# Performance work log

Hardware: AMD Instinct MI355X
Metric: run time of the kernel (lower is better)

The kernel has to match this reference:

```python
import jax, jax.numpy as jnp
import numpy as np

B, S, D, H = 4, 2048, 512, 8
DH = D // H  # 64


def setup_inputs() -> dict:
    key = jax.random.key(0)
    ks = jax.random.split(key, 7)
    scale = 1.0 / np.sqrt(D)
    return {
        "in_query": jax.random.normal(ks[0], (B, S, D), dtype=jnp.float32),
        "in_key": jax.random.normal(ks[1], (B, S, D), dtype=jnp.float32),
        "in_value": jax.random.normal(ks[2], (B, S, D), dtype=jnp.float32),
        "W_q": jax.random.normal(ks[3], (D, D), dtype=jnp.float32) * scale,
        "W_k": jax.random.normal(ks[4], (D, D), dtype=jnp.float32) * scale,
        "W_v": jax.random.normal(ks[5], (D, D), dtype=jnp.float32) * scale,
        "W_out": jax.random.normal(ks[6], (D, D), dtype=jnp.float32) * scale,
    }


def _split_heads(x):
    # [B, S, D] -> [B, H, S, DH]
    return x.reshape(B, S, H, DH).transpose(0, 2, 1, 3)


def reference(in_query, in_key, in_value, W_q, W_k, W_v, W_out):
    q = _split_heads(in_query @ W_q)   # [B,H,S,DH]
    k = _split_heads(in_key @ W_k)
    v = _split_heads(in_value @ W_v)
    scores = jnp.einsum("bhqd,bhkd->bhqk", q, k) / jnp.sqrt(jnp.float32(DH))
    attn = jax.nn.softmax(scores, axis=-1)  # dropout p=0 -> identity
    out = jnp.einsum("bhqk,bhkd->bhqd", attn, v)  # [B,H,S,DH]
    out = out.transpose(0, 2, 1, 3).reshape(B, S, D)
    return out @ W_out
```

## Files before the change

### kernel.cpp

```cpp
#include <hip/hip_runtime.h>
#include <hip/hip_bf16.h>
#include <cstdint>
#include <cstddef>


typedef __bf16 bf16;
typedef __attribute__((ext_vector_type(8))) __bf16 bf16x8;
typedef __attribute__((ext_vector_type(4))) __bf16 bf16x4;
typedef __attribute__((ext_vector_type(4))) float floatx4;

#define MFMA16(a, b, c) __builtin_amdgcn_mfma_f32_16x16x32_bf16(a, b, c, 0, 0, 0)

#define GLD16(gp, lp)                                              \
  __builtin_amdgcn_global_load_lds(                                \
      (const __attribute__((address_space(1))) unsigned int*)(gp), \
      (__attribute__((address_space(3))) unsigned int*)(lp), 16, 0, 0)

__device__ __forceinline__ void split2(float x, bf16& hi, bf16& lo) {
  hi = (bf16)x;
  lo = (bf16)(x - (float)hi);
}

__global__ __launch_bounds__(256) void k_split_w(
    const float* __restrict__ Wq, const float* __restrict__ Wk,
    const float* __restrict__ Wv, const float* __restrict__ Wo,
    bf16* __restrict__ wt_hi, bf16* __restrict__ wt_lo) {
  __shared__ float tile[64][65];
  const int w = blockIdx.z;
  const float* W = (w == 0) ? Wq : (w == 1) ? Wk : (w == 2) ? Wv : Wo;
  const int kb = blockIdx.y * 64, nb = blockIdx.x * 64;
  const int tid = threadIdx.x;
  const int col = tid & 63, rbase = tid >> 6;
#pragma unroll
  for (int i = 0; i < 16; i++) {
    int row = rbase + i * 4;
    tile[row][col] = W[(size_t)(kb + row) * 512 + nb + col];
  }
  __syncthreads();
#pragma unroll
  for (int i = 0; i < 16; i++) {
    int nrow = rbase + i * 4;
    float v = tile[col][nrow];
    bf16 hi, lo;
    split2(v, hi, lo);
    size_t o = (size_t)w * 262144 + (size_t)(nb + nrow) * 512 + (kb + col);
    wt_hi[o] = hi;
    wt_lo[o] = lo;
  }
}

__global__ __launch_bounds__(256) void k_proj_qkv(
    const float* __restrict__ Xq, const float* __restrict__ Xk,
    const float* __restrict__ Xv,
    const bf16* __restrict__ wt_hi, const bf16* __restrict__ wt_lo,
    bf16* __restrict__ Q_hi, bf16* __restrict__ Q_lo,
    bf16* __restrict__ K, bf16* __restrict__ Vt) {
  const int P = blockIdx.x;
  const int c_all = P >> 5, within = P & 31;
  const int n_idx = within >> 3, i8 = within & 7;
  const int which = c_all >> 3;
  const int g = ((c_all & 7) << 3) | i8;
  const int m0 = g * 128, n0 = n_idx * 128;

  const float* X = (which == 0) ? Xq : (which == 1) ? Xk : Xv;
  const uint8_t* Bhb = (const uint8_t*)(wt_hi + (size_t)which * 262144);
  const uint8_t* Blb = (const uint8_t*)(wt_lo + (size_t)which * 262144);
  const uint8_t* Xb = (const uint8_t*)X;
  const int tid = threadIdx.x, wave = tid >> 6, lane = tid & 63;
  const int l15 = lane & 15, l4 = lane >> 4;
  const int Am0 = (wave & 1) * 64, Bn0 = (wave >> 1) * 64;

  __shared__ float sA[128 * 32];
  __shared__ bf16 sBh[128 * 32], sBl[128 * 32];

  int aoff[4], adst[4];
#pragma unroll
  for (int p = 0; p < 4; p++) {
    int slot = p * 256 + tid;
    int row = slot >> 3, phys = slot & 7, lg = phys ^ (row & 7);
    aoff[p] = (m0 + row) * 2048 + lg * 16;
    adst[p] = slot * 16;
  }
  int boff[2], bdst[2];
#pragma unroll
  for (int p = 0; p < 2; p++) {
    int slot = p * 256 + tid;
    int row = slot >> 2, phys = slot & 3, lg = phys ^ (row & 3);
    boff[p] = (n0 + row) * 1024 + lg * 16;
    bdst[p] = slot * 16;
  }

  floatx4 acc[4][4];
#pragma unroll
  for (int i = 0; i < 4; i++)
#pragma unroll
    for (int j = 0; j < 4; j++) acc[i][j] = {0.f, 0.f, 0.f, 0.f};

  for (int kb = 0; kb < 512; kb += 32) {
    __syncthreads();
#pragma unroll
    for (int p = 0; p < 4; p++) GLD16(Xb + aoff[p] + kb * 4, (char*)sA + adst[p]);
#pragma unroll
    for (int p = 0; p < 2; p++) {
      GLD16(Bhb + boff[p] + kb * 2, (char*)sBh + bdst[p]);
      GLD16(Blb + boff[p] + kb * 2, (char*)sBl + bdst[p]);
    }
    __syncthreads();

    bf16x8 ah[4], al[4];
#pragma unroll
    for (int mt = 0; mt < 4; mt++) {
      int row = Am0 + mt * 16 + l15, r7 = row & 7;
      const float* f0 = (const float*)((const char*)sA + row * 128 + (((2 * l4) ^ r7) * 16));
      const float* f1 = (const float*)((const char*)sA + row * 128 + (((2 * l4 + 1) ^ r7) * 16));
#pragma unroll
      for (int j = 0; j < 4; j++) {
        bf16 h, l;
        split2(f0[j], h, l);
        ah[mt][j] = h; al[mt][j] = l;
        split2(f1[j], h, l);
        ah[mt][4 + j] = h; al[mt][4 + j] = l;
      }
    }
#pragma unroll
    for (int nt = 0; nt < 4; nt++) {
      int row = Bn0 + nt * 16 + l15, r3 = row & 3;
      bf16x8 bh = *(const bf16x8*)((const char*)sBh + row * 64 + ((l4 ^ r3) * 16));
      bf16x8 bl = *(const bf16x8*)((const char*)sBl + row * 64 + ((l4 ^ r3) * 16));
#pragma unroll
      for (int mt = 0; mt < 4; mt++) {
        acc[mt][nt] = MFMA16(ah[mt], bh, acc[mt][nt]);
        acc[mt][nt] = MFMA16(ah[mt], bl, acc[mt][nt]);
        acc[mt][nt] = MFMA16(al[mt], bh, acc[mt][nt]);
      }
    }
  }

  const float scale = (which == 0) ? 0.125f : (which == 1) ? 1.44269504f : 1.0f;
#pragma unroll
  for (int mt = 0; mt < 4; mt++) {
#pragma unroll
    for (int nt = 0; nt < 4; nt++) {
      int m_base = m0 + Am0 + mt * 16 + l4 * 4;
      int n = n0 + Bn0 + nt * 16 + l15;
      int h = (n >> 6) & 7, d = n & 63;
      if (which == 2) {
        int kbase = m_base & 2047, b = m_base >> 11;
        int a32 = kbase & ~31, v = (kbase >> 2) & 7;
        int sbase = a32 + 8 * (v & 3) + 4 * (v >> 2);
        bf16x4 pv;
#pragma unroll
        for (int r = 0; r < 4; r++) pv[r] = (bf16)acc[mt][nt][r];
        *(bf16x4*)&Vt[((size_t)(b * 8 + h) * 64 + d) * 2048 + sbase] = pv;
      } else {
#pragma unroll
        for (int r = 0; r < 4; r++) {
          int m = m_base + r;
          int b = m >> 11, s = m & 2047;
          float v = acc[mt][nt][r] * scale;
          size_t o = ((size_t)(b * 8 + h) * 2048 + s) * 64 + d;
          if (which == 0) {
            bf16 hi, lo;
            split2(v, hi, lo);
            Q_hi[o] = hi; Q_lo[o] = lo;
          } else {
            K[o] = (bf16)v;
          }
        }
      }
    }
  }
}

__global__ __launch_bounds__(256, 2) void k_flash(
    const bf16* __restrict__ Q_hi, const bf16* __restrict__ Q_lo,
    const bf16* __restrict__ K, const bf16* __restrict__ Vt,
    bf16* __restrict__ O_hi, bf16* __restrict__ O_lo) {
  const int P = blockIdx.x;
  const int hi4 = P >> 8, rem = P & 255;
  const int qt = rem >> 3;
  const int bh = hi4 * 8 + (rem & 7);
  const int b = bh >> 3, h = bh & 7;
  const int tid = threadIdx.x, wave = tid >> 6, lane = tid & 63;
  const int l15 = lane & 15, l4 = lane >> 4;
  const int q0 = qt * 64;

  __shared__ char smem[33792];
  bf16* sK = (bf16*)smem;
  bf16* sV = (bf16*)(smem + 16384);
  float* lbuf = (float*)(smem + 32768);

  bf16x8 qh[4][2], ql[4][2];
#pragma unroll
  for (int nt = 0; nt < 4; nt++) {
    const bf16* ph = Q_hi + ((size_t)bh * 2048 + q0 + nt * 16 + l15) * 64 + l4 * 8;
    const bf16* pl = Q_lo + ((size_t)bh * 2048 + q0 + nt * 16 + l15) * 64 + l4 * 8;
    qh[nt][0] = *(const bf16x8*)ph;
    qh[nt][1] = *(const bf16x8*)(ph + 32);
    ql[nt][0] = *(const bf16x8*)pl;
    ql[nt][1] = *(const bf16x8*)(pl + 32);
  }

  const uint8_t* Kb = (const uint8_t*)K + (size_t)bh * 2048 * 128;
  const uint8_t* Vb = (const uint8_t*)Vt + (size_t)bh * 64 * 4096;
  int koff[4], voff[4], dst[4];
#pragma unroll
  for (int p = 0; p < 4; p++) {
    int slot = p * 256 + tid;
    {
      int row = slot >> 3, phys = slot & 7, lg = phys ^ (row & 7);
      koff[p] = row * 128 + lg * 16;
    }
    {
      int row = slot >> 4, phys = slot & 15, lg = phys ^ (row & 15);
      voff[p] = row * 4096 + lg * 16;
    }
    dst[p] = slot * 16;
  }

  float lp[4] = {0.f, 0.f, 0.f, 0.f};
  floatx4 oacc[4][4];
#pragma unroll
  for (int i = 0; i < 4; i++)
#pragma unroll
    for (int j = 0; j < 4; j++) oacc[i][j] = {0.f, 0.f, 0.f, 0.f};

  for (int j0 = 0; j0 < 2048; j0 += 128) {
    __syncthreads();
#pragma unroll
    for (int p = 0; p < 4; p++) {
      GLD16(Kb + (size_t)j0 * 128 + koff[p], (char*)sK + dst[p]);
      GLD16(Vb + (size_t)j0 * 2 + voff[p], (char*)sV + dst[p]);
    }
    __syncthreads();

    floatx4 sc[2][4];
#pragma unroll
    for (int kt = 0; kt < 2; kt++)
#pragma unroll
      for (int nt = 0; nt < 4; nt++)
        sc[kt][nt] = {-24.f, -24.f, -24.f, -24.f};
#pragma unroll
    for (int kt = 0; kt < 2; kt++) {
      int row = wave * 32 + kt * 16 + l15;
      int r7 = row & 7;
#pragma unroll
      for (int ks = 0; ks < 2; ks++) {
        bf16x8 kh = *(const bf16x8*)((const char*)sK +
                                     (row * 128 + (((ks * 4 + l4) ^ r7) * 16)));
#pragma unroll
        for (int nt = 0; nt < 4; nt++) {
          sc[kt][nt] = MFMA16(kh, qh[nt][ks], sc[kt][nt]);
          sc[kt][nt] = MFMA16(kh, ql[nt][ks], sc[kt][nt]);
        }
      }
    }

    bf16x8 pf[4];
#pragma unroll
    for (int nt = 0; nt < 4; nt++) {
#pragma unroll
      for (int r = 0; r < 4; r++) {
        float p0 = __builtin_amdgcn_exp2f(sc[0][nt][r]);
        float p1 = __builtin_amdgcn_exp2f(sc[1][nt][r]);
        lp[nt] += p0 + p1;
        pf[nt][r] = (bf16)p0;
        pf[nt][4 + r] = (bf16)p1;
      }
    }

#pragma unroll
    for (int nt = 0; nt < 4; nt++) {
      int row = nt * 16 + l15;
      bf16x8 bv = *(const bf16x8*)((const char*)sV +
                                   (row * 256 + (((wave * 4 + l4) ^ l15) * 16)));
#pragma unroll
      for (int mq = 0; mq < 4; mq++)
        oacc[mq][nt] = MFMA16(pf[mq], bv, oacc[mq][nt]);
    }
  }

#pragma unroll
  for (int nt = 0; nt < 4; nt++) {
    lp[nt] += __shfl_xor(lp[nt], 16, 64);
    lp[nt] += __shfl_xor(lp[nt], 32, 64);
  }
  __syncthreads();
  if (l4 == 0) {
#pragma unroll
    for (int nt = 0; nt < 4; nt++) lbuf[wave * 64 + nt * 16 + l15] = lp[nt];
  }
  floatx4* red = (floatx4*)smem;
#pragma unroll
  for (int phase = 0; phase < 2; phase++) {
    if (wave >= 1) {
#pragma unroll
      for (int i = 0; i < 8; i++) {
        int mq = phase * 2 + (i >> 2);
        red[(wave - 1) * 512 + i * 64 + lane] = oacc[mq][i & 3];
      }
    }
    __syncthreads();
    if (wave == 0) {
#pragma unroll
      for (int i = 0; i < 8; i++) {
        int mq = phase * 2 + (i >> 2);
        oacc[mq][i & 3] += red[i * 64 + lane] + red[512 + i * 64 + lane] +
                           red[1024 + i * 64 + lane];
      }
    }
    __syncthreads();
  }
  if (wave == 0) {
    float lt[4];
#pragma unroll
    for (int nt = 0; nt < 4; nt++)
      lt[nt] = lbuf[nt * 16 + l15] + lbuf[64 + nt * 16 + l15] +
               lbuf[128 + nt * 16 + l15] + lbuf[192 + nt * 16 + l15];
    float rl[4][4];
#pragma unroll
    for (int mq = 0; mq < 4; mq++)
#pragma unroll
      for (int r = 0; r < 4; r++)
        rl[mq][r] = 1.0f / __shfl(lt[mq], (lane & 48) | (l4 * 4 + r), 64);
#pragma unroll
    for (int mq = 0; mq < 4; mq++) {
#pragma unroll
      for (int nt = 0; nt < 4; nt++) {
#pragma unroll
        for (int r = 0; r < 4; r++) {
          float v = oacc[mq][nt][r] * rl[mq][r];
          int gs = q0 + mq * 16 + l4 * 4 + r;
          int gd = h * 64 + nt * 16 + l15;
          size_t o = ((size_t)b * 2048 + gs) * 512 + gd;
          bf16 hi, lo;
          split2(v, hi, lo);
          O_hi[o] = hi;
          O_lo[o] = lo;
        }
      }
    }
  }
}

__global__ __launch_bounds__(256) void k_proj_out(
    const bf16* __restrict__ O_hi, const bf16* __restrict__ O_lo,
    const bf16* __restrict__ wt_hi, const bf16* __restrict__ wt_lo,
    float* __restrict__ out) {
  const int P = blockIdx.x;
  const int c = P >> 5, within = P & 31;
  const int n_idx = within >> 3, i8 = within & 7;
  const int g = (c << 3) | i8;
  const int m0 = g * 128, n0 = n_idx * 128;

  const uint8_t* Ahb = (const uint8_t*)O_hi;
  const uint8_t* Alb = (const uint8_t*)O_lo;
  const uint8_t* Bhb = (const uint8_t*)(wt_hi + (size_t)3 * 262144);
  const uint8_t* Blb = (const uint8_t*)(wt_lo + (size_t)3 * 262144);
  const int tid = threadIdx.x, wave = tid >> 6, lane = tid & 63;
  const int l15 = lane & 15, l4 = lane >> 4;
  const int Am0 = (wave & 1) * 64, Bn0 = (wave >> 1) * 64;

  __shared__ bf16 sAh[128 * 32], sAl[128 * 32];
  __shared__ bf16 sBh[128 * 32], sBl[128 * 32];

  int aoff[2], boff[2], dst[2];
#pragma unroll
  for (int p = 0; p < 2; p++) {
    int slot = p * 256 + tid;
    int row = slot >> 2, phys = slot & 3, lg = phys ^ (row & 3);
    aoff[p] = (m0 + row) * 1024 + lg * 16;
    boff[p] = (n0 + row) * 1024 + lg * 16;
    dst[p] = slot * 16;
  }

  floatx4 acc[4][4];
#pragma unroll
  for (int i = 0; i < 4; i++)
#pragma unroll
    for (int j = 0; j < 4; j++) acc[i][j] = {0.f, 0.f, 0.f, 0.f};

  for (int kb = 0; kb < 512; kb += 32) {
    __syncthreads();
#pragma unroll
    for (int p = 0; p < 2; p++) {
      GLD16(Ahb + aoff[p] + kb * 2, (char*)sAh + dst[p]);
      GLD16(Alb + aoff[p] + kb * 2, (char*)sAl + dst[p]);
      GLD16(Bhb + boff[p] + kb * 2, (char*)sBh + dst[p]);
      GLD16(Blb + boff[p] + kb * 2, (char*)sBl + dst[p]);
    }
    __syncthreads();

    bf16x8 ah[4], al[4];
#pragma unroll
    for (int mt = 0; mt < 4; mt++) {
      int row = Am0 + mt * 16 + l15, r3 = row & 3;
      ah[mt] = *(const bf16x8*)((const char*)sAh + row * 64 + ((l4 ^ r3) * 16));
      al[mt] = *(const bf16x8*)((const char*)sAl + row * 64 + ((l4 ^ r3) * 16));
    }
#pragma unroll
    for (int nt = 0; nt < 4; nt++) {
      int row = Bn0 + nt * 16 + l15, r3 = row & 3;
      bf16x8 bh = *(const bf16x8*)((const char*)sBh + row * 64 + ((l4 ^ r3) * 16));
      bf16x8 bl = *(const bf16x8*)((const char*)sBl + row * 64 + ((l4 ^ r3) * 16));
#pragma unroll
      for (int mt = 0; mt < 4; mt++) {
        acc[mt][nt] = MFMA16(ah[mt], bh, acc[mt][nt]);
        acc[mt][nt] = MFMA16(ah[mt], bl, acc[mt][nt]);
        acc[mt][nt] = MFMA16(al[mt], bh, acc[mt][nt]);
      }
    }
  }
#pragma unroll
  for (int mt = 0; mt < 4; mt++) {
#pragma unroll
    for (int nt = 0; nt < 4; nt++) {
#pragma unroll
      for (int r = 0; r < 4; r++) {
        int m = m0 + Am0 + mt * 16 + l4 * 4 + r;
        int n = n0 + Bn0 + nt * 16 + l15;
        out[(size_t)m * 512 + n] = acc[mt][nt][r];
      }
    }
  }
}

extern "C" void kernel_launch(void* const* d_in, const int* in_sizes, int n_in,
                              void* d_out, int out_size, void* d_ws, size_t ws_size,
                              hipStream_t stream) {
  (void)in_sizes; (void)n_in; (void)out_size; (void)ws_size;
  const float* Xq = (const float*)d_in[0];
  const float* Xk = (const float*)d_in[1];
  const float* Xv = (const float*)d_in[2];
  const float* Wq = (const float*)d_in[3];
  const float* Wk = (const float*)d_in[4];
  const float* Wv = (const float*)d_in[5];
  const float* Wo = (const float*)d_in[6];
  float* out = (float*)d_out;

  char* ws = (char*)d_ws;
  size_t off = 0;
  auto alloc = [&](size_t n) {
    void* p = ws + off;
    off += (n + 255) & ~(size_t)255;
    return p;
  };
  const size_t NW = 4 * 262144;
  const size_t NE = 4194304;
  bf16* wt_hi = (bf16*)alloc(NW * 2);
  bf16* wt_lo = (bf16*)alloc(NW * 2);
  bf16* Qh = (bf16*)alloc(NE * 2);
  bf16* Ql = (bf16*)alloc(NE * 2);
  bf16* Kk = (bf16*)alloc(NE * 2);
  bf16* Vt = (bf16*)alloc(NE * 2);
  bf16* Oh = (bf16*)alloc(NE * 2);
  bf16* Ol = (bf16*)alloc(NE * 2);

  k_split_w<<<dim3(8, 8, 4), dim3(256), 0, stream>>>(Wq, Wk, Wv, Wo, wt_hi, wt_lo);
  k_proj_qkv<<<dim3(768), dim3(256), 0, stream>>>(Xq, Xk, Xv, wt_hi, wt_lo,
                                                  Qh, Ql, Kk, Vt);
  k_flash<<<dim3(1024), dim3(256), 0, stream>>>(Qh, Ql, Kk, Vt, Oh, Ol);
  k_proj_out<<<dim3(256), dim3(256), 0, stream>>>(Oh, Ol, wt_hi, wt_lo, out);
}
```

Before: 222.5 us.

## Double-buffer LDS tiles in projection and flash kernels to overlap loads

Adds a second shared-memory buffer to the QKV projection, flash attention and output projection kernels. The next K-slice or KV tile is prefetched with async global-to-LDS loads while the current tile is computed on, which removes one barrier per iteration and hides load latency. This doubles LDS use, and the flash kernel now needs about 65 KB per block, which may reduce occupancy. It also relies on the single trailing barrier to make the async LDS writes visible before the next iteration reads them.

```diff
diff --git a/kernel.cpp b/kernel.cpp
--- a/kernel.cpp
+++ b/kernel.cpp
@@ -49,7 +49,7 @@
   }
 }
 
-__global__ __launch_bounds__(256) void k_proj_qkv(
+__global__ __launch_bounds__(256, 2) void k_proj_qkv(
     const float* __restrict__ Xq, const float* __restrict__ Xk,
     const float* __restrict__ Xv,
     const bf16* __restrict__ wt_hi, const bf16* __restrict__ wt_lo,
@@ -70,8 +70,8 @@
   const int l15 = lane & 15, l4 = lane >> 4;
   const int Am0 = (wave & 1) * 64, Bn0 = (wave >> 1) * 64;
 
-  __shared__ float sA[128 * 32];
-  __shared__ bf16 sBh[128 * 32], sBl[128 * 32];
+  __shared__ float sA[2][128 * 32];
+  __shared__ bf16 sBh[2][128 * 32], sBl[2][128 * 32];
 
   int aoff[4], adst[4];
 #pragma unroll
@@ -96,23 +96,38 @@
 #pragma unroll
     for (int j = 0; j < 4; j++) acc[i][j] = {0.f, 0.f, 0.f, 0.f};
 
+#pragma unroll
+  for (int p = 0; p < 4; p++) GLD16(Xb + aoff[p], (char*)sA[0] + adst[p]);
+#pragma unroll
+  for (int p = 0; p < 2; p++) {
+    GLD16(Bhb + boff[p], (char*)sBh[0] + bdst[p]);
+    GLD16(Blb + boff[p], (char*)sBl[0] + bdst[p]);
+  }
+  __syncthreads();
+
+  int cur = 0;
   for (int kb = 0; kb < 512; kb += 32) {
-    __syncthreads();
-#pragma unroll
-    for (int p = 0; p < 4; p++) GLD16(Xb + aoff[p] + kb * 4, (char*)sA + adst[p]);
-#pragma unroll
-    for (int p = 0; p < 2; p++) {
-      GLD16(Bhb + boff[p] + kb * 2, (char*)sBh + bdst[p]);
-      GLD16(Blb + boff[p] + kb * 2, (char*)sBl + bdst[p]);
-    }
-    __syncthreads();
+    if (kb + 32 < 512) {
+      const int nx = cur ^ 1, nkb = kb + 32;
+#pragma unroll
+      for (int p = 0; p < 4; p++)
+        GLD16(Xb + aoff[p] + nkb * 4, (char*)sA[nx] + adst[p]);
+#pragma unroll
+      for (int p = 0; p < 2; p++) {
+        GLD16(Bhb + boff[p] + nkb * 2, (char*)sBh[nx] + bdst[p]);
+        GLD16(Blb + boff[p] + nkb * 2, (char*)sBl[nx] + bdst[p]);
+      }
+    }
+    const char* cA = (const char*)sA[cur];
+    const char* cBh = (const char*)sBh[cur];
+    const char* cBl = (const char*)sBl[cur];
 
     bf16x8 ah[4], al[4];
 #pragma unroll
     for (int mt = 0; mt < 4; mt++) {
       int row = Am0 + mt * 16 + l15, r7 = row & 7;
-      const float* f0 = (const float*)((const char*)sA + row * 128 + (((2 * l4) ^ r7) * 16));
-      const float* f1 = (const float*)((const char*)sA + row * 128 + (((2 * l4 + 1) ^ r7) * 16));
+      const float* f0 = (const float*)(cA + row * 128 + (((2 * l4) ^ r7) * 16));
+      const float* f1 = (const float*)(cA + row * 128 + (((2 * l4 + 1) ^ r7) * 16));
 #pragma unroll
       for (int j = 0; j < 4; j++) {
         bf16 h, l;
@@ -125,8 +140,8 @@
 #pragma unroll
     for (int nt = 0; nt < 4; nt++) {
       int row = Bn0 + nt * 16 + l15, r3 = row & 3;
-      bf16x8 bh = *(const bf16x8*)((const char*)sBh + row * 64 + ((l4 ^ r3) * 16));
-      bf16x8 bl = *(const bf16x8*)((const char*)sBl + row * 64 + ((l4 ^ r3) * 16));
+      bf16x8 bh = *(const bf16x8*)(cBh + row * 64 + ((l4 ^ r3) * 16));
+      bf16x8 bl = *(const bf16x8*)(cBl + row * 64 + ((l4 ^ r3) * 16));
 #pragma unroll
       for (int mt = 0; mt < 4; mt++) {
         acc[mt][nt] = MFMA16(ah[mt], bh, acc[mt][nt]);
@@ -134,6 +149,8 @@
         acc[mt][nt] = MFMA16(al[mt], bh, acc[mt][nt]);
       }
     }
+    __syncthreads();
+    cur ^= 1;
   }
 
   const float scale = (which == 0) ? 0.125f : (which == 1) ? 1.44269504f : 1.0f;
@@ -185,10 +202,31 @@
   const int l15 = lane & 15, l4 = lane >> 4;
   const int q0 = qt * 64;
 
-  __shared__ char smem[33792];
-  bf16* sK = (bf16*)smem;
-  bf16* sV = (bf16*)(smem + 16384);
-  float* lbuf = (float*)(smem + 32768);
+  __shared__ char smem[2 * 32768 + 1024];
+  float* lbuf = (float*)(smem + 65536);
+
+  const uint8_t* Kb = (const uint8_t*)K + (size_t)bh * 2048 * 128;
+  const uint8_t* Vb = (const uint8_t*)Vt + (size_t)bh * 64 * 4096;
+  int koff[4], voff[4], dst[4];
+#pragma unroll
+  for (int p = 0; p < 4; p++) {
+    int slot = p * 256 + tid;
+    {
+      int row = slot >> 3, phys = slot & 7, lg = phys ^ (row & 7);
+      koff[p] = row * 128 + lg * 16;
+    }
+    {
+      int row = slot >> 4, phys = slot & 15, lg = phys ^ (row & 15);
+      voff[p] = row * 4096 + lg * 16;
+    }
+    dst[p] = slot * 16;
+  }
+
+#pragma unroll
+  for (int p = 0; p < 4; p++) {
+    GLD16(Kb + koff[p], smem + dst[p]);
+    GLD16(Vb + voff[p], smem + 16384 + dst[p]);
+  }
 
   bf16x8 qh[4][2], ql[4][2];
 #pragma unroll
@@ -201,23 +239,6 @@
     ql[nt][1] = *(const bf16x8*)(pl + 32);
   }
 
-  const uint8_t* Kb = (const uint8_t*)K + (size_t)bh * 2048 * 128;
-  const uint8_t* Vb = (const uint8_t*)Vt + (size_t)bh * 64 * 4096;
-  int koff[4], voff[4], dst[4];
-#pragma unroll
-  for (int p = 0; p < 4; p++) {
-    int slot = p * 256 + tid;
-    {
-      int row = slot >> 3, phys = slot & 7, lg = phys ^ (row & 7);
-      koff[p] = row * 128 + lg * 16;
-    }
-    {
-      int row = slot >> 4, phys = slot & 15, lg = phys ^ (row & 15);
-      voff[p] = row * 4096 + lg * 16;
-    }
-    dst[p] = slot * 16;
-  }
-
   float lp[4] = {0.f, 0.f, 0.f, 0.f};
   floatx4 oacc[4][4];
 #pragma unroll
@@ -225,14 +246,21 @@
 #pragma unroll
     for (int j = 0; j < 4; j++) oacc[i][j] = {0.f, 0.f, 0.f, 0.f};
 
+  __syncthreads();
+
+  int cur = 0;
   for (int j0 = 0; j0 < 2048; j0 += 128) {
-    __syncthreads();
-#pragma unroll
-    for (int p = 0; p < 4; p++) {
-      GLD16(Kb + (size_t)j0 * 128 + koff[p], (char*)sK + dst[p]);
-      GLD16(Vb + (size_t)j0 * 2 + voff[p], (char*)sV + dst[p]);
-    }
-    __syncthreads();
+    if (j0 + 128 < 2048) {
+      char* nb = smem + (cur ^ 1) * 32768;
+      const size_t nj = (size_t)(j0 + 128);
+#pragma unroll
+      for (int p = 0; p < 4; p++) {
+        GLD16(Kb + nj * 128 + koff[p], nb + dst[p]);
+        GLD16(Vb + nj * 2 + voff[p], nb + 16384 + dst[p]);
+      }
+    }
+    const char* sK = smem + cur * 32768;
+    const char* sV = sK + 16384;
 
     floatx4 sc[2][4];
 #pragma unroll
@@ -246,8 +274,7 @@
       int r7 = row & 7;
 #pragma unroll
       for (int ks = 0; ks < 2; ks++) {
-        bf16x8 kh = *(const bf16x8*)((const char*)sK +
-                                     (row * 128 + (((ks * 4 + l4) ^ r7) * 16)));
+        bf16x8 kh = *(const bf16x8*)(sK + (row * 128 + (((ks * 4 + l4) ^ r7) * 16)));
 #pragma unroll
         for (int nt = 0; nt < 4; nt++) {
           sc[kt][nt] = MFMA16(kh, qh[nt][ks], sc[kt][nt]);
@@ -272,12 +299,14 @@
 #pragma unroll
     for (int nt = 0; nt < 4; nt++) {
       int row = nt * 16 + l15;
-      bf16x8 bv = *(const bf16x8*)((const char*)sV +
-                                   (row * 256 + (((wave * 4 + l4) ^ l15) * 16)));
+      bf16x8 bv = *(const bf16x8*)(sV + (row * 256 + (((wave * 4 + l4) ^ l15) * 16)));
 #pragma unroll
       for (int mq = 0; mq < 4; mq++)
         oacc[mq][nt] = MFMA16(pf[mq], bv, oacc[mq][nt]);
     }
+
+    __syncthreads();
+    cur ^= 1;
   }
 
 #pragma unroll
@@ -285,7 +314,6 @@
     lp[nt] += __shfl_xor(lp[nt], 16, 64);
     lp[nt] += __shfl_xor(lp[nt], 32, 64);
   }
-  __syncthreads();
   if (l4 == 0) {
 #pragma unroll
     for (int nt = 0; nt < 4; nt++) lbuf[wave * 64 + nt * 16 + l15] = lp[nt];
@@ -343,7 +371,7 @@
   }
 }
 
-__global__ __launch_bounds__(256) void k_proj_out(
+__global__ __launch_bounds__(256, 2) void k_proj_out(
     const bf16* __restrict__ O_hi, const bf16* __restrict__ O_lo,
     const bf16* __restrict__ wt_hi, const bf16* __restrict__ wt_lo,
     float* __restrict__ out) {
@@ -361,8 +389,8 @@
   const int l15 = lane & 15, l4 = lane >> 4;
   const int Am0 = (wave & 1) * 64, Bn0 = (wave >> 1) * 64;
 
-  __shared__ bf16 sAh[128 * 32], sAl[128 * 32];
-  __shared__ bf16 sBh[128 * 32], sBl[128 * 32];
+  __shared__ bf16 sAh[2][128 * 32], sAl[2][128 * 32];
+  __shared__ bf16 sBh[2][128 * 32], sBl[2][128 * 32];
 
   int aoff[2], boff[2], dst[2];
 #pragma unroll
@@ -380,29 +408,44 @@
 #pragma unroll
     for (int j = 0; j < 4; j++) acc[i][j] = {0.f, 0.f, 0.f, 0.f};
 
+#pragma unroll
+  for (int p = 0; p < 2; p++) {
+    GLD16(Ahb + aoff[p], (char*)sAh[0] + dst[p]);
+    GLD16(Alb + aoff[p], (char*)sAl[0] + dst[p]);
+    GLD16(Bhb + boff[p], (char*)sBh[0] + dst[p]);
+    GLD16(Blb + boff[p], (char*)sBl[0] + dst[p]);
+  }
+  __syncthreads();
+
+  int cur = 0;
   for (int kb = 0; kb < 512; kb += 32) {
-    __syncthreads();
-#pragma unroll
-    for (int p = 0; p < 2; p++) {
-      GLD16(Ahb + aoff[p] + kb * 2, (char*)sAh + dst[p]);
-      GLD16(Alb + aoff[p] + kb * 2, (char*)sAl + dst[p]);
-      GLD16(Bhb + boff[p] + kb * 2, (char*)sBh + dst[p]);
-      GLD16(Blb + boff[p] + kb * 2, (char*)sBl + dst[p]);
-    }
-    __syncthreads();
+    if (kb + 32 < 512) {
+      const int nx = cur ^ 1, nkb = kb + 32;
+#pragma unroll
+      for (int p = 0; p < 2; p++) {
+        GLD16(Ahb + aoff[p] + nkb * 2, (char*)sAh[nx] + dst[p]);
+        GLD16(Alb + aoff[p] + nkb * 2, (char*)sAl[nx] + dst[p]);
+        GLD16(Bhb + boff[p] + nkb * 2, (char*)sBh[nx] + dst[p]);
+        GLD16(Blb + boff[p] + nkb * 2, (char*)sBl[nx] + dst[p]);
+      }
+    }
+    const char* cAh = (const char*)sAh[cur];
+    const char* cAl = (const char*)sAl[cur];
+    const char* cBh = (const char*)sBh[cur];
+    const char* cBl = (const char*)sBl[cur];
 
     bf16x8 ah[4], al[4];
 #pragma unroll
     for (int mt = 0; mt < 4; mt++) {
       int row = Am0 + mt * 16 + l15, r3 = row & 3;
-      ah[mt] = *(const bf16x8*)((const char*)sAh + row * 64 + ((l4 ^ r3) * 16));
-      al[mt] = *(const bf16x8*)((const char*)sAl + row * 64 + ((l4 ^ r3) * 16));
+      ah[mt] = *(const bf16x8*)(cAh + row * 64 + ((l4 ^ r3) * 16));
+      al[mt] = *(const bf16x8*)(cAl + row * 64 + ((l4 ^ r3) * 16));
     }
 #pragma unroll
     for (int nt = 0; nt < 4; nt++) {
       int row = Bn0 + nt * 16 + l15, r3 = row & 3;
-      bf16x8 bh = *(const bf16x8*)((const char*)sBh + row * 64 + ((l4 ^ r3) * 16));
-      bf16x8 bl = *(const bf16x8*)((const char*)sBl + row * 64 + ((l4 ^ r3) * 16));
+      bf16x8 bh = *(const bf16x8*)(cBh + row * 64 + ((l4 ^ r3) * 16));
+      bf16x8 bl = *(const bf16x8*)(cBl + row * 64 + ((l4 ^ r3) * 16));
 #pragma unroll
       for (int mt = 0; mt < 4; mt++) {
         acc[mt][nt] = MFMA16(ah[mt], bh, acc[mt][nt]);
@@ -410,6 +453,8 @@
         acc[mt][nt] = MFMA16(al[mt], bh, acc[mt][nt]);
       }
     }
+    __syncthreads();
+    cur ^= 1;
   }
 #pragma unroll
   for (int mt = 0; mt < 4; mt++) {
```

Measured after the change: 222.2 us. No clear change (-0.1%).

## Replace LDS staging with direct global-to-register loads in all GEMM and flash kernels

Applied to the files above, without the earlier changes.

Removes the global_load_lds staging into shared memory and the paired barriers in the QKV projection, flash attention and output projection kernels. Each lane now loads its MFMA operands straight from global memory into registers, relying on L1/L2 caches for reuse across waves. The loop is unrolled by two, and launch bounds are raised to request two blocks per CU. This drops synchronisation and LDS traffic but loses explicit data sharing between waves, so redundant global and cache traffic grows and uncoalesced per-lane loads may stall the MFMA pipeline.

```diff
diff --git a/kernel.cpp b/kernel.cpp
--- a/kernel.cpp
+++ b/kernel.cpp
@@ -10,11 +10,6 @@
 typedef __attribute__((ext_vector_type(4))) float floatx4;
 
 #define MFMA16(a, b, c) __builtin_amdgcn_mfma_f32_16x16x32_bf16(a, b, c, 0, 0, 0)
-
-#define GLD16(gp, lp)                                              \
-  __builtin_amdgcn_global_load_lds(                                \
-      (const __attribute__((address_space(1))) unsigned int*)(gp), \
-      (__attribute__((address_space(3))) unsigned int*)(lp), 16, 0, 0)
 
 __device__ __forceinline__ void split2(float x, bf16& hi, bf16& lo) {
   hi = (bf16)x;
@@ -49,7 +44,7 @@
   }
 }
 
-__global__ __launch_bounds__(256) void k_proj_qkv(
+__global__ __launch_bounds__(256, 2) void k_proj_qkv(
     const float* __restrict__ Xq, const float* __restrict__ Xk,
     const float* __restrict__ Xv,
     const bf16* __restrict__ wt_hi, const bf16* __restrict__ wt_lo,
@@ -70,24 +65,19 @@
   const int l15 = lane & 15, l4 = lane >> 4;
   const int Am0 = (wave & 1) * 64, Bn0 = (wave >> 1) * 64;
 
-  __shared__ float sA[128 * 32];
-  __shared__ bf16 sBh[128 * 32], sBl[128 * 32];
-
-  int aoff[4], adst[4];
-#pragma unroll
-  for (int p = 0; p < 4; p++) {
-    int slot = p * 256 + tid;
-    int row = slot >> 3, phys = slot & 7, lg = phys ^ (row & 7);
-    aoff[p] = (m0 + row) * 2048 + lg * 16;
-    adst[p] = slot * 16;
-  }
-  int boff[2], bdst[2];
-#pragma unroll
-  for (int p = 0; p < 2; p++) {
-    int slot = p * 256 + tid;
-    int row = slot >> 2, phys = slot & 3, lg = phys ^ (row & 3);
-    boff[p] = (n0 + row) * 1024 + lg * 16;
-    bdst[p] = slot * 16;
+  const uint8_t* aptr[4];
+  const uint8_t* bhp[4];
+  const uint8_t* blp[4];
+#pragma unroll
+  for (int mt = 0; mt < 4; mt++) {
+    int row = m0 + Am0 + mt * 16 + l15;
+    aptr[mt] = Xb + (size_t)row * 2048 + l4 * 32;
+  }
+#pragma unroll
+  for (int nt = 0; nt < 4; nt++) {
+    int row = n0 + Bn0 + nt * 16 + l15;
+    bhp[nt] = Bhb + (size_t)row * 1024 + l4 * 16;
+    blp[nt] = Blb + (size_t)row * 1024 + l4 * 16;
   }
 
   floatx4 acc[4][4];
@@ -96,23 +86,13 @@
 #pragma unroll
     for (int j = 0; j < 4; j++) acc[i][j] = {0.f, 0.f, 0.f, 0.f};
 
+#pragma unroll 2
   for (int kb = 0; kb < 512; kb += 32) {
-    __syncthreads();
-#pragma unroll
-    for (int p = 0; p < 4; p++) GLD16(Xb + aoff[p] + kb * 4, (char*)sA + adst[p]);
-#pragma unroll
-    for (int p = 0; p < 2; p++) {
-      GLD16(Bhb + boff[p] + kb * 2, (char*)sBh + bdst[p]);
-      GLD16(Blb + boff[p] + kb * 2, (char*)sBl + bdst[p]);
-    }
-    __syncthreads();
-
     bf16x8 ah[4], al[4];
 #pragma unroll
     for (int mt = 0; mt < 4; mt++) {
-      int row = Am0 + mt * 16 + l15, r7 = row & 7;
-      const float* f0 = (const float*)((const char*)sA + row * 128 + (((2 * l4) ^ r7) * 16));
-      const float* f1 = (const float*)((const char*)sA + row * 128 + (((2 * l4 + 1) ^ r7) * 16));
+      floatx4 f0 = *(const floatx4*)(aptr[mt] + kb * 4);
+      floatx4 f1 = *(const floatx4*)(aptr[mt] + kb * 4 + 16);
 #pragma unroll
       for (int j = 0; j < 4; j++) {
         bf16 h, l;
@@ -124,9 +104,8 @@
     }
 #pragma unroll
     for (int nt = 0; nt < 4; nt++) {
-      int row = Bn0 + nt * 16 + l15, r3 = row & 3;
-      bf16x8 bh = *(const bf16x8*)((const char*)sBh + row * 64 + ((l4 ^ r3) * 16));
-      bf16x8 bl = *(const bf16x8*)((const char*)sBl + row * 64 + ((l4 ^ r3) * 16));
+      bf16x8 bh = *(const bf16x8*)(bhp[nt] + kb * 2);
+      bf16x8 bl = *(const bf16x8*)(blp[nt] + kb * 2);
 #pragma unroll
       for (int mt = 0; mt < 4; mt++) {
         acc[mt][nt] = MFMA16(ah[mt], bh, acc[mt][nt]);
@@ -185,10 +164,8 @@
   const int l15 = lane & 15, l4 = lane >> 4;
   const int q0 = qt * 64;
 
-  __shared__ char smem[33792];
-  bf16* sK = (bf16*)smem;
-  bf16* sV = (bf16*)(smem + 16384);
-  float* lbuf = (float*)(smem + 32768);
+  __shared__ char smem[24576 + 1024];
+  float* lbuf = (float*)(smem + 24576);
 
   bf16x8 qh[4][2], ql[4][2];
 #pragma unroll
@@ -203,20 +180,6 @@
 
   const uint8_t* Kb = (const uint8_t*)K + (size_t)bh * 2048 * 128;
   const uint8_t* Vb = (const uint8_t*)Vt + (size_t)bh * 64 * 4096;
-  int koff[4], voff[4], dst[4];
-#pragma unroll
-  for (int p = 0; p < 4; p++) {
-    int slot = p * 256 + tid;
-    {
-      int row = slot >> 3, phys = slot & 7, lg = phys ^ (row & 7);
-      koff[p] = row * 128 + lg * 16;
-    }
-    {
-      int row = slot >> 4, phys = slot & 15, lg = phys ^ (row & 15);
-      voff[p] = row * 4096 + lg * 16;
-    }
-    dst[p] = slot * 16;
-  }
 
   float lp[4] = {0.f, 0.f, 0.f, 0.f};
   floatx4 oacc[4][4];
@@ -225,15 +188,8 @@
 #pragma unroll
     for (int j = 0; j < 4; j++) oacc[i][j] = {0.f, 0.f, 0.f, 0.f};
 
+#pragma unroll 2
   for (int j0 = 0; j0 < 2048; j0 += 128) {
-    __syncthreads();
-#pragma unroll
-    for (int p = 0; p < 4; p++) {
-      GLD16(Kb + (size_t)j0 * 128 + koff[p], (char*)sK + dst[p]);
-      GLD16(Vb + (size_t)j0 * 2 + voff[p], (char*)sV + dst[p]);
-    }
-    __syncthreads();
-
     floatx4 sc[2][4];
 #pragma unroll
     for (int kt = 0; kt < 2; kt++)
@@ -242,12 +198,10 @@
         sc[kt][nt] = {-24.f, -24.f, -24.f, -24.f};
 #pragma unroll
     for (int kt = 0; kt < 2; kt++) {
-      int row = wave * 32 + kt * 16 + l15;
-      int r7 = row & 7;
+      int key = j0 + wave * 32 + kt * 16 + l15;
 #pragma unroll
       for (int ks = 0; ks < 2; ks++) {
-        bf16x8 kh = *(const bf16x8*)((const char*)sK +
-                                     (row * 128 + (((ks * 4 + l4) ^ r7) * 16)));
+        bf16x8 kh = *(const bf16x8*)(Kb + (size_t)key * 128 + (ks * 4 + l4) * 16);
 #pragma unroll
         for (int nt = 0; nt < 4; nt++) {
           sc[kt][nt] = MFMA16(kh, qh[nt][ks], sc[kt][nt]);
@@ -272,8 +226,8 @@
 #pragma unroll
     for (int nt = 0; nt < 4; nt++) {
       int row = nt * 16 + l15;
-      bf16x8 bv = *(const bf16x8*)((const char*)sV +
-                                   (row * 256 + (((wave * 4 + l4) ^ l15) * 16)));
+      bf16x8 bv = *(const bf16x8*)(Vb + (size_t)row * 4096 + j0 * 2 +
+                                   (wave * 4 + l4) * 16);
 #pragma unroll
       for (int mq = 0; mq < 4; mq++)
         oacc[mq][nt] = MFMA16(pf[mq], bv, oacc[mq][nt]);
@@ -285,7 +239,6 @@
     lp[nt] += __shfl_xor(lp[nt], 16, 64);
     lp[nt] += __shfl_xor(lp[nt], 32, 64);
   }
-  __syncthreads();
   if (l4 == 0) {
 #pragma unroll
     for (int nt = 0; nt < 4; nt++) lbuf[wave * 64 + nt * 16 + l15] = lp[nt];
@@ -343,7 +296,7 @@
   }
 }
 
-__global__ __launch_bounds__(256) void k_proj_out(
+__global__ __launch_bounds__(256, 2) void k_proj_out(
     const bf16* __restrict__ O_hi, const bf16* __restrict__ O_lo,
     const bf16* __restrict__ wt_hi, const bf16* __restrict__ wt_lo,
     float* __restrict__ out) {
@@ -361,17 +314,21 @@
   const int l15 = lane & 15, l4 = lane >> 4;
   const int Am0 = (wave & 1) * 64, Bn0 = (wave >> 1) * 64;
 
-  __shared__ bf16 sAh[128 * 32], sAl[128 * 32];
-  __shared__ bf16 sBh[128 * 32], sBl[128 * 32];
-
-  int aoff[2], boff[2], dst[2];
-#pragma unroll
-  for (int p = 0; p < 2; p++) {
-    int slot = p * 256 + tid;
-    int row = slot >> 2, phys = slot & 3, lg = phys ^ (row & 3);
-    aoff[p] = (m0 + row) * 1024 + lg * 16;
-    boff[p] = (n0 + row) * 1024 + lg * 16;
-    dst[p] = slot * 16;
+  const uint8_t* ahp[4];
+  const uint8_t* alp[4];
+  const uint8_t* bhp[4];
+  const uint8_t* blp[4];
+#pragma unroll
+  for (int mt = 0; mt < 4; mt++) {
+    int row = m0 + Am0 + mt * 16 + l15;
+    ahp[mt] = Ahb + (size_t)row * 1024 + l4 * 16;
+    alp[mt] = Alb + (size_t)row * 1024 + l4 * 16;
+  }
+#pragma unroll
+  for (int nt = 0; nt < 4; nt++) {
+    int row = n0 + Bn0 + nt * 16 + l15;
+    bhp[nt] = Bhb + (size_t)row * 1024 + l4 * 16;
+    blp[nt] = Blb + (size_t)row * 1024 + l4 * 16;
   }
 
   floatx4 acc[4][4];
@@ -380,29 +337,18 @@
 #pragma unroll
     for (int j = 0; j < 4; j++) acc[i][j] = {0.f, 0.f, 0.f, 0.f};
 
+#pragma unroll 2
   for (int kb = 0; kb < 512; kb += 32) {
-    __syncthreads();
-#pragma unroll
-    for (int p = 0; p < 2; p++) {
-      GLD16(Ahb + aoff[p] + kb * 2, (char*)sAh + dst[p]);
-      GLD16(Alb + aoff[p] + kb * 2, (char*)sAl + dst[p]);
-      GLD16(Bhb + boff[p] + kb * 2, (char*)sBh + dst[p]);
-      GLD16(Blb + boff[p] + kb * 2, (char*)sBl + dst[p]);
-    }
-    __syncthreads();
-
     bf16x8 ah[4], al[4];
 #pragma unroll
     for (int mt = 0; mt < 4; mt++) {
-      int row = Am0 + mt * 16 + l15, r3 = row & 3;
-      ah[mt] = *(const bf16x8*)((const char*)sAh + row * 64 + ((l4 ^ r3) * 16));
-      al[mt] = *(const bf16x8*)((const char*)sAl + row * 64 + ((l4 ^ r3) * 16));
-    }
-#pragma unroll
-    for (int nt = 0; nt < 4; nt++) {
-      int row = Bn0 + nt * 16 + l15, r3 = row & 3;
-      bf16x8 bh = *(const bf16x8*)((const char*)sBh + row * 64 + ((l4 ^ r3) * 16));
-      bf16x8 bl = *(const bf16x8*)((const char*)sBl + row * 64 + ((l4 ^ r3) * 16));
+      ah[mt] = *(const bf16x8*)(ahp[mt] + kb * 2);
+      al[mt] = *(const bf16x8*)(alp[mt] + kb * 2);
+    }
+#pragma unroll
+    for (int nt = 0; nt < 4; nt++) {
+      bf16x8 bh = *(const bf16x8*)(bhp[nt] + kb * 2);
+      bf16x8 bl = *(const bf16x8*)(blp[nt] + kb * 2);
 #pragma unroll
       for (int mt = 0; mt < 4; mt++) {
         acc[mt][nt] = MFMA16(ah[mt], bh, acc[mt][nt]);
```

Measured after the change: 297.6 us. 33.7% more time.
